# Kernel optimization log

Measured on AMD Instinct MI355X. Metric: run time of the kernel, lower is better.

The kernel has to match this reference:

```python
import jax, jax.numpy as jnp
import numpy as np


def _ramp_filter(sino):
    # Ram-Lak ramp filter along detector columns (last axis), applied in Fourier
    # space. Equivalent to projector.filter_projections, vectorized over batch.
    n = sino.shape[-1]
    ramp = (2.0 * jnp.abs(jnp.fft.fftfreq(n))).astype(sino.dtype)  # [C]
    f = jnp.fft.fft(sino, axis=-1)
    return jnp.real(jnp.fft.ifft(f * ramp, axis=-1)).astype(sino.dtype)


def _fbp(sino):
    # sino: [B, V, R, C] -> image [B, R, C, C]
    B, V, R, C = sino.shape
    filt = _ramp_filter(sino)
    npix = C
    half = (npix - 1) / 2.0
    coords = jnp.arange(npix, dtype=sino.dtype) - half
    X = coords[None, :]          # image x, broadcasts to [npix, npix]
    Y = coords[:, None]          # image y
    angles = jnp.linspace(0.0, np.pi, V, endpoint=False).astype(sino.dtype)
    dcenter = (C - 1) / 2.0

    def body(acc, inputs):
        proj, theta = inputs                      # proj: [B, R, C]
        t = X * jnp.cos(theta) + Y * jnp.sin(theta) + dcenter  # [npix, npix]
        t = jnp.clip(t, 0.0, C - 1)
        i0 = jnp.floor(t).astype(jnp.int32)
        i1 = jnp.minimum(i0 + 1, C - 1)
        w = (t - i0).astype(proj.dtype)
        g0 = proj[:, :, i0]                       # gather -> [B, R, npix, npix]
        g1 = proj[:, :, i1]
        return acc + g0 * (1.0 - w) + g1 * w, None

    init = jnp.zeros((B, R, npix, npix), sino.dtype)
    projT = jnp.moveaxis(filt, 1, 0)              # [V, B, R, C]
    acc, _ = jax.lax.scan(body, init, (projT, angles))
    img = acc * (np.pi / V)
    return jnp.maximum(img, 0.0)                  # img[img < 0] = 0


def setup_inputs() -> dict:
    key = jax.random.key(0)
    B, V, R, C = 2, 180, 32, 512
    sino = jax.random.normal(key, (B, V, R, C), dtype=jnp.float32)
    return {"sino": sino}


def reference(sino):
    return _fbp(sino)
```

## Files before the change

### kernel.cpp

```cpp
#include <hip/hip_runtime.h>
#include <hip/hip_fp16.h>
#include <math.h>

#ifndef M_PI
#define M_PI 3.14159265358979323846
#endif

#define BB 2
#define VV 180
#define RR 32
#define CC 512
#define NPIX 512

#define PADL 106
#define PW 724
#define TCEN 362

#define SH3 8
#define CHP 2
#define NCHP 45

#define SH 16
#define CH2 6
#define NCHUNK2 30

#define H4_OFF 2048
#define TAB_OFF 6144
#define FILT_OFF 2048

__global__ void precompute_kernel(float* __restrict__ ws) {
    int j = blockIdx.x * blockDim.x + threadIdx.x;
    if (j < 512) {
        float s = 0.f;
        for (int m = 1; m < 512; ++m) {
            int p = (m * j) & 511;
            float ang = (float)(2.0 * M_PI / 512.0) * (float)p;
            int mm = m < 512 - m ? m : 512 - m;
            float ramp = 2.0f * (float)mm * (1.0f / 512.0f);
            s += ramp * cosf(ang);
        }
        s *= (1.0f / 512.0f);
        s *= (float)(M_PI / (double)VV);
        ws[j] = s;
        ws[j + 512] = s;
    }
    if (j < VV) {
        float th = (float)((double)j * M_PI / 180.0);
        float c = cosf(th), sn = sinf(th);
        ws[1024 + j] = c;
        ws[1024 + 180 + j] = sn;
        ws[1408 + 2 * j] = c;
        ws[1408 + 2 * j + 1] = sn;
    }
}

__global__ void precompute_h4_kernel(float* __restrict__ ws) {
    int x = blockIdx.x * blockDim.x + threadIdx.x;
    if (x < 1024) {
        float4 h4;
        h4.x = ws[x];
        h4.y = ws[(x - 1) & 1023];
        h4.z = ws[(x - 2) & 1023];
        h4.w = ws[(x - 3) & 1023];
        *(float4*)(ws + H4_OFF + 4 * x) = h4;
    }
}

__global__ __launch_bounds__(128) void conv_table_kernel(const float* __restrict__ sino,
                                                         const float* __restrict__ ws,
                                                         unsigned int* __restrict__ table) {
    __shared__ float rows_s[16 * 512];
    __shared__ float4 h4_s[1024];
    int t = threadIdx.x;
    int blk = blockIdx.x;
    int bv = blk >> 1;
    int half = blk & 1;
    int b = bv / 180;
    int v = bv - b * 180;

    const float4* src4 = (const float4*)(sino + (((size_t)bv * 32) + (size_t)half * 16) * 512);
    float4* rows4 = (float4*)rows_s;
    for (int i = t; i < 2048; i += 128) rows4[i] = src4[i];
    const float4* h4g = (const float4*)(ws + H4_OFF);
    for (int i = t; i < 1024; i += 128) h4_s[i] = h4g[i];
    __syncthreads();

    int wave = t >> 6;
    int lane = t & 63;
    int row0 = wave * 8;

    float acc[8][8];
#pragma unroll
    for (int j = 0; j < 8; ++j)
#pragma unroll
        for (int i = 0; i < 8; ++i) acc[j][i] = 0.f;

    for (int k = 0; k < 512; k += 4) {
        float4 rv[8];
#pragma unroll
        for (int j = 0; j < 8; ++j)
            rv[j] = *(const float4*)&rows_s[(row0 + j) * 512 + k];
        float4 hq[8];
#pragma unroll
        for (int i = 0; i < 8; ++i)
            hq[i] = h4_s[lane - k + 512 + 64 * i];
#pragma unroll
        for (int j = 0; j < 8; ++j) {
#pragma unroll
            for (int i = 0; i < 8; ++i) {
                float a = acc[j][i];
                a = fmaf(rv[j].x, hq[i].x, a);
                a = fmaf(rv[j].y, hq[i].y, a);
                a = fmaf(rv[j].z, hq[i].z, a);
                a = fmaf(rv[j].w, hq[i].w, a);
                acc[j][i] = a;
            }
        }
    }

    __syncthreads();
#pragma unroll
    for (int j = 0; j < 8; ++j)
#pragma unroll
        for (int i = 0; i < 8; ++i)
            rows_s[(row0 + j) * 512 + lane + 64 * i] = acc[j][i];
    __syncthreads();

    int p = (v < 90) ? v : v - 90;
    int word = (v < 90) ? 0 : 1;
    for (int jj = 0; jj < 16; ++jj) {
        const float* fr = rows_s + jj * 512;
        int slice = b * 32 + half * 16 + jj;
        unsigned int* trow = table + (((size_t)slice * 90 + p) * PW) * 2 + word;
        for (int cx = t; cx < PW; cx += 128) {
            int s0 = cx - PADL;
            int i0 = min(max(s0, 0), 511);
            int i1 = min(max(s0 + 1, 0), 511);
            float f0 = fr[i0];
            float f1 = fr[i1];
            __half h0 = __float2half_rn(f0);
            __half h1 = __float2half_rn(f1);
            __half hd = __float2half_rn(__half2float(h1) - __half2float(h0));
            unsigned int packed = ((unsigned int)__half_as_ushort(hd) << 16) |
                                  (unsigned int)__half_as_ushort(h0);
            trow[(size_t)cx * 2] = packed;
        }
    }
}

static __device__ inline float2 unpack_h2(unsigned int u) {
    __half2 h = *reinterpret_cast<__half2*>(&u);
    return __half22float2(h);
}

__global__ __launch_bounds__(256, 6) void backproj_pair_kernel(const uint2* __restrict__ tab,
                                                               const float2* __restrict__ trigp,
                                                               float* __restrict__ out) {
    __shared__ uint2 pbuf[CHP * PW];
    __shared__ float2 trig_s[90];
    int t = threadIdx.x;
    int slice = blockIdx.y;
    int strip = blockIdx.x;
    int y0 = strip * SH3;
    const uint2* tslice = tab + (size_t)slice * (90 * PW);

    for (int i = t; i < 90; i += 256) trig_s[i] = trigp[i];

    float xc = (float)t + 0.5f;

    float acc0[SH3], acc1[SH3], acc2[SH3], acc3[SH3];
#pragma unroll
    for (int j = 0; j < SH3; ++j) { acc0[j] = 0.f; acc1[j] = 0.f; acc2[j] = 0.f; acc3[j] = 0.f; }

    for (int chunk = 0; chunk < NCHP; ++chunk) {
        __syncthreads();
        const float4* src = (const float4*)(tslice + chunk * (CHP * PW));
        float4* dst = (float4*)pbuf;
        for (int i = t; i < (CHP * PW) / 2; i += 256) dst[i] = src[i];
        __syncthreads();
#pragma unroll
        for (int pa = 0; pa < CHP; ++pa) {
            float2 cs = trig_s[chunk * CHP + pa];
            const uint2* pb = pbuf + pa * PW + TCEN;
#pragma unroll
            for (int j = 0; j < SH3; ++j) {
                float ycj = (float)(y0 + j) + 0.5f;
                float ysm  = fmaf(ycj, cs.y, -0.5f);
                float yccm = fmaf(-ycj, cs.x, -0.5f);
                float ua  = fmaf(xc, cs.x, ysm);
                float ub  = fmaf(xc, cs.y, yccm);
                float fla = floorf(ua);
                float flb = floorf(ub);
                int ma  = (int)fla;
                int mb  = (int)flb;
                float ra = ua - fla;
                float rb = ub - flb;
                int mma = -2 - ma;
                int mmb = -2 - mb;
                float rma = 1.0f - ra;
                float rmb = 1.0f - rb;
                uint2 qa  = pb[ma];
                uint2 qma = pb[mma];
                uint2 qb  = pb[mb];
                uint2 qmb = pb[mmb];
                float2 av  = unpack_h2(qa.x);
                float2 aw  = unpack_h2(qa.y);
                acc0[j] += fmaf(ra,  av.y, av.x);
                acc1[j] += fmaf(ra,  aw.y, aw.x);
                float2 mav = unpack_h2(qma.x);
                float2 maw = unpack_h2(qma.y);
                acc2[j] += fmaf(rma, mav.y, mav.x);
                acc3[j] += fmaf(rma, maw.y, maw.x);
                float2 bv  = unpack_h2(qb.x);
                float2 bw  = unpack_h2(qb.y);
                acc1[j] += fmaf(rb,  bv.y, bv.x);
                acc2[j] += fmaf(rb,  bw.y, bw.x);
                float2 mbv = unpack_h2(qmb.x);
                float2 mbw = unpack_h2(qmb.y);
                acc3[j] += fmaf(rmb, mbv.y, mbv.x);
                acc0[j] += fmaf(rmb, mbw.y, mbw.x);
            }
        }
    }

    int px = 256 + t;
    size_t sbase = (size_t)slice * (512 * 512);
#pragma unroll
    for (int j = 0; j < SH3; ++j) {
        int py = 256 + y0 + j;
        float v0 = acc0[j], v1 = acc1[j], v2 = acc2[j], v3 = acc3[j];
        out[sbase + (size_t)py * 512 + px]                   = v0 > 0.f ? v0 : 0.f;
        out[sbase + (size_t)px * 512 + (511 - py)]           = v1 > 0.f ? v1 : 0.f;
        out[sbase + (size_t)(511 - py) * 512 + (511 - px)]   = v2 > 0.f ? v2 : 0.f;
        out[sbase + (size_t)(511 - px) * 512 + py]           = v3 > 0.f ? v3 : 0.f;
    }
}

__global__ __launch_bounds__(128) void conv_kernel(const float* __restrict__ sino,
                                                   const float* __restrict__ ws,
                                                   float* __restrict__ filt) {
    __shared__ float rows_s[16 * 512];
    __shared__ float h_s[1024];
    int t = threadIdx.x;
    int blk = blockIdx.x;
    int bv = blk >> 1;
    int half = blk & 1;
    int b = bv / 180;
    int v = bv - b * 180;

    const float4* src4 = (const float4*)(sino + (((size_t)bv * 32) + (size_t)half * 16) * 512);
    float4* rows4 = (float4*)rows_s;
    for (int i = t; i < 2048; i += 128) rows4[i] = src4[i];
    for (int i = t; i < 1024; i += 128) h_s[i] = ws[i];
    __syncthreads();

    int wave = t >> 6;
    int lane = t & 63;
    int row0 = wave * 8;

    float acc[8][8];
#pragma unroll
    for (int j = 0; j < 8; ++j)
#pragma unroll
        for (int i = 0; i < 8; ++i) acc[j][i] = 0.f;

    for (int k = 0; k < 512; k += 4) {
        float4 rv[8];
#pragma unroll
        for (int j = 0; j < 8; ++j)
            rv[j] = *(const float4*)&rows_s[(row0 + j) * 512 + k];
#pragma unroll
        for (int u = 0; u < 4; ++u) {
            float hv[8];
            int base = lane - (k + u) + 512;
#pragma unroll
            for (int i = 0; i < 8; ++i) hv[i] = h_s[base + 64 * i];
#pragma unroll
            for (int j = 0; j < 8; ++j) {
                float rj = (u == 0) ? rv[j].x : (u == 1) ? rv[j].y : (u == 2) ? rv[j].z : rv[j].w;
#pragma unroll
                for (int i = 0; i < 8; ++i) acc[j][i] = fmaf(rj, hv[i], acc[j][i]);
            }
        }
    }

#pragma unroll
    for (int j = 0; j < 8; ++j) {
        int r = half * 16 + row0 + j;
        float* dst = filt + (((size_t)b * 32 + r) * 180 + v) * 512;
#pragma unroll
        for (int i = 0; i < 8; ++i) dst[lane + 64 * i] = acc[j][i];
    }
}

__global__ __launch_bounds__(256) void backproj_kernel(const float* __restrict__ filt,
                                                       const float* __restrict__ trig,
                                                       float* __restrict__ out) {
    __shared__ float2 pbuf[CH2][PW];
    __shared__ float trig_s[360];
    int t = threadIdx.x;
    int slice = blockIdx.y;
    int strip = blockIdx.x;
    int y0 = strip * SH;
    int lane = t & 63;
    int wave = t >> 6;
    int x0 = wave * 128;
    const float* slice_p = filt + (size_t)slice * (180 * 512);

    for (int i = t; i < 360; i += 256) trig_s[i] = trig[i];

    float xc0 = (float)(x0 + lane) - 255.5f;
    float xc1 = xc0 + 64.0f;
    float yb0 = (float)y0 - 255.5f;

    float acc[2][SH];
#pragma unroll
    for (int g = 0; g < 2; ++g)
#pragma unroll
        for (int j = 0; j < SH; ++j) acc[g][j] = 0.f;

    for (int chunk = 0; chunk < NCHUNK2; ++chunk) {
        int v0 = chunk * CH2;
        __syncthreads();
#pragma unroll 1
        for (int a = 0; a < CH2; ++a) {
            const float* prow = slice_p + (v0 + a) * 512;
            for (int cx = t; cx < PW; cx += 256) {
                int s0 = cx - PADL;
                int i0 = min(max(s0, 0), 511);
                int i1 = min(max(s0 + 1, 0), 511);
                float f0 = prow[i0];
                float d = prow[i1] - f0;
                float m = (float)(cx - TCEN);
                pbuf[a][cx] = make_float2(fmaf(-m, d, f0), d);
            }
        }
        __syncthreads();
#pragma unroll 1
        for (int a = 0; a < CH2; ++a) {
            float cth = trig_s[v0 + a];
            float sth = trig_s[180 + v0 + a];
            float ybase = fmaf(yb0, sth, 255.5f + (float)PADL - (float)TCEN);
            float t0 = fmaf(xc0, cth, ybase);
            float t1 = fmaf(xc1, cth, ybase);
            const char* pb = (const char*)pbuf;
            int aoff = a * (PW * 8) + TCEN * 8;
#pragma unroll
            for (int j = 0; j < SH; ++j) {
                int m0 = (int)floorf(t0);
                float2 g0 = *(const float2*)(pb + (m0 * 8 + aoff));
                acc[0][j] = fmaf(t0, g0.y, acc[0][j]) + g0.x;
                t0 += sth;

                int m1 = (int)floorf(t1);
                float2 g1 = *(const float2*)(pb + (m1 * 8 + aoff));
                acc[1][j] = fmaf(t1, g1.y, acc[1][j]) + g1.x;
                t1 += sth;
            }
        }
    }

    size_t obase = ((size_t)slice * 512 + (size_t)y0) * 512;
#pragma unroll
    for (int j = 0; j < SH; ++j) {
        float v0o = acc[0][j];
        float v1o = acc[1][j];
        out[obase + (size_t)j * 512 + x0 + lane] = v0o > 0.f ? v0o : 0.f;
        out[obase + (size_t)j * 512 + x0 + 64 + lane] = v1o > 0.f ? v1o : 0.f;
    }
}

extern "C" void kernel_launch(void* const* d_in, const int* in_sizes, int n_in,
                              void* d_out, int out_size, void* d_ws, size_t ws_size,
                              hipStream_t stream) {
    const float* sino = (const float*)d_in[0];
    float* out = (float*)d_out;
    float* ws = (float*)d_ws;

    size_t tableWords = (size_t)64 * 90 * PW * 2;
    size_t needed = ((size_t)TAB_OFF + tableWords) * 4;

    precompute_kernel<<<2, 256, 0, stream>>>(ws);
    if (ws_size >= needed) {
        unsigned int* table = (unsigned int*)(ws + TAB_OFF);
        precompute_h4_kernel<<<4, 256, 0, stream>>>(ws);
        conv_table_kernel<<<720, 128, 0, stream>>>(sino, ws, table);
        backproj_pair_kernel<<<dim3(32, 64), 256, 0, stream>>>((const uint2*)table,
                                                               (const float2*)(ws + 1408), out);
    } else {
        float* filt = ws + FILT_OFF;
        conv_kernel<<<720, 128, 0, stream>>>(sino, ws, filt);
        backproj_kernel<<<dim3(32, 64), 256, 0, stream>>>(filt, ws + 1024, out);
    }
}
```

Baseline: 682.1 us.

## Repack half table layout for packed FMA and widen conv block

Changes the half-precision table layout so each uint2 holds the two angles' base values in one word and their deltas in the other. The backprojection inner loop can then use two-wide packed FMAs (v_pk_fma_f32) with split accumulators, which are recombined once at output. The conv-table kernel moves from 128 to 256 threads with 4 rows per wave, which raises parallelism and cuts register pressure. Table writes become 16-bit scattered stores, which may cost more write bandwidth.

After: 1.100 ms. 61.3% more time.

```diff
diff --git a/kernel.cpp b/kernel.cpp
--- a/kernel.cpp
+++ b/kernel.cpp
@@ -27,6 +27,23 @@
 #define H4_OFF 2048
 #define TAB_OFF 6144
 #define FILT_OFF 2048
+
+typedef float f32x2 __attribute__((ext_vector_type(2)));
+
+static __device__ __forceinline__ f32x2 mk2(float a, float b) {
+    f32x2 r; r.x = a; r.y = b; return r;
+}
+
+static __device__ __forceinline__ float2 unpack_h2(unsigned int u) {
+    __half2 h = *reinterpret_cast<__half2*>(&u);
+    return __half22float2(h);
+}
+
+static __device__ __forceinline__ f32x2 sample2(float r, uint2 q) {
+    float2 f0 = unpack_h2(q.x);
+    float2 d  = unpack_h2(q.y);
+    return __builtin_elementwise_fma(mk2(r, r), mk2(d.x, d.y), mk2(f0.x, f0.y));
+}
 
 __global__ void precompute_kernel(float* __restrict__ ws) {
     int j = blockIdx.x * blockDim.x + threadIdx.x;
@@ -66,7 +83,7 @@
     }
 }
 
-__global__ __launch_bounds__(128) void conv_table_kernel(const float* __restrict__ sino,
+__global__ __launch_bounds__(256) void conv_table_kernel(const float* __restrict__ sino,
                                                          const float* __restrict__ ws,
                                                          unsigned int* __restrict__ table) {
     __shared__ float rows_s[16 * 512];
@@ -80,32 +97,32 @@
 
     const float4* src4 = (const float4*)(sino + (((size_t)bv * 32) + (size_t)half * 16) * 512);
     float4* rows4 = (float4*)rows_s;
-    for (int i = t; i < 2048; i += 128) rows4[i] = src4[i];
+    for (int i = t; i < 2048; i += 256) rows4[i] = src4[i];
     const float4* h4g = (const float4*)(ws + H4_OFF);
-    for (int i = t; i < 1024; i += 128) h4_s[i] = h4g[i];
+    for (int i = t; i < 1024; i += 256) h4_s[i] = h4g[i];
     __syncthreads();
 
     int wave = t >> 6;
     int lane = t & 63;
-    int row0 = wave * 8;
-
-    float acc[8][8];
-#pragma unroll
-    for (int j = 0; j < 8; ++j)
+    int row0 = wave * 4;
+
+    float acc[4][8];
+#pragma unroll
+    for (int j = 0; j < 4; ++j)
 #pragma unroll
         for (int i = 0; i < 8; ++i) acc[j][i] = 0.f;
 
     for (int k = 0; k < 512; k += 4) {
-        float4 rv[8];
-#pragma unroll
-        for (int j = 0; j < 8; ++j)
+        float4 rv[4];
+#pragma unroll
+        for (int j = 0; j < 4; ++j)
             rv[j] = *(const float4*)&rows_s[(row0 + j) * 512 + k];
         float4 hq[8];
 #pragma unroll
         for (int i = 0; i < 8; ++i)
             hq[i] = h4_s[lane - k + 512 + 64 * i];
 #pragma unroll
-        for (int j = 0; j < 8; ++j) {
+        for (int j = 0; j < 4; ++j) {
 #pragma unroll
             for (int i = 0; i < 8; ++i) {
                 float a = acc[j][i];
@@ -120,19 +137,19 @@
 
     __syncthreads();
 #pragma unroll
-    for (int j = 0; j < 8; ++j)
+    for (int j = 0; j < 4; ++j)
 #pragma unroll
         for (int i = 0; i < 8; ++i)
             rows_s[(row0 + j) * 512 + lane + 64 * i] = acc[j][i];
     __syncthreads();
 
     int p = (v < 90) ? v : v - 90;
-    int word = (v < 90) ? 0 : 1;
+    int sh = (v < 90) ? 0 : 1;
     for (int jj = 0; jj < 16; ++jj) {
         const float* fr = rows_s + jj * 512;
         int slice = b * 32 + half * 16 + jj;
-        unsigned int* trow = table + (((size_t)slice * 90 + p) * PW) * 2 + word;
-        for (int cx = t; cx < PW; cx += 128) {
+        unsigned short* trow = (unsigned short*)(table + (((size_t)slice * 90 + p) * PW) * 2);
+        for (int cx = t; cx < PW; cx += 256) {
             int s0 = cx - PADL;
             int i0 = min(max(s0, 0), 511);
             int i1 = min(max(s0 + 1, 0), 511);
@@ -141,16 +158,10 @@
             __half h0 = __float2half_rn(f0);
             __half h1 = __float2half_rn(f1);
             __half hd = __float2half_rn(__half2float(h1) - __half2float(h0));
-            unsigned int packed = ((unsigned int)__half_as_ushort(hd) << 16) |
-                                  (unsigned int)__half_as_ushort(h0);
-            trow[(size_t)cx * 2] = packed;
-        }
-    }
-}
-
-static __device__ inline float2 unpack_h2(unsigned int u) {
-    __half2 h = *reinterpret_cast<__half2*>(&u);
-    return __half22float2(h);
+            trow[(size_t)cx * 4 + sh]     = __half_as_ushort(h0);
+            trow[(size_t)cx * 4 + 2 + sh] = __half_as_ushort(hd);
+        }
+    }
 }
 
 __global__ __launch_bounds__(256, 6) void backproj_pair_kernel(const uint2* __restrict__ tab,
@@ -168,9 +179,12 @@
 
     float xc = (float)t + 0.5f;
 
-    float acc0[SH3], acc1[SH3], acc2[SH3], acc3[SH3];
-#pragma unroll
-    for (int j = 0; j < SH3; ++j) { acc0[j] = 0.f; acc1[j] = 0.f; acc2[j] = 0.f; acc3[j] = 0.f; }
+    f32x2 accA[SH3], accM[SH3], accB[SH3], accC[SH3];
+#pragma unroll
+    for (int j = 0; j < SH3; ++j) {
+        accA[j] = mk2(0.f, 0.f); accM[j] = mk2(0.f, 0.f);
+        accB[j] = mk2(0.f, 0.f); accC[j] = mk2(0.f, 0.f);
+    }
 
     for (int chunk = 0; chunk < NCHP; ++chunk) {
         __syncthreads();
@@ -203,22 +217,10 @@
                 uint2 qma = pb[mma];
                 uint2 qb  = pb[mb];
                 uint2 qmb = pb[mmb];
-                float2 av  = unpack_h2(qa.x);
-                float2 aw  = unpack_h2(qa.y);
-                acc0[j] += fmaf(ra,  av.y, av.x);
-                acc1[j] += fmaf(ra,  aw.y, aw.x);
-                float2 mav = unpack_h2(qma.x);
-                float2 maw = unpack_h2(qma.y);
-                acc2[j] += fmaf(rma, mav.y, mav.x);
-                acc3[j] += fmaf(rma, maw.y, maw.x);
-                float2 bv  = unpack_h2(qb.x);
-                float2 bw  = unpack_h2(qb.y);
-                acc1[j] += fmaf(rb,  bv.y, bv.x);
-                acc2[j] += fmaf(rb,  bw.y, bw.x);
-                float2 mbv = unpack_h2(qmb.x);
-                float2 mbw = unpack_h2(qmb.y);
-                acc3[j] += fmaf(rmb, mbv.y, mbv.x);
-                acc0[j] += fmaf(rmb, mbw.y, mbw.x);
+                accA[j] += sample2(ra,  qa);
+                accM[j] += sample2(rma, qma);
+                accB[j] += sample2(rb,  qb);
+                accC[j] += sample2(rmb, qmb);
             }
         }
     }
@@ -228,7 +230,10 @@
 #pragma unroll
     for (int j = 0; j < SH3; ++j) {
         int py = 256 + y0 + j;
-        float v0 = acc0[j], v1 = acc1[j], v2 = acc2[j], v3 = acc3[j];
+        float v0 = accA[j].x + accC[j].y;
+        float v1 = accA[j].y + accB[j].x;
+        float v2 = accM[j].x + accB[j].y;
+        float v3 = accM[j].y + accC[j].x;
         out[sbase + (size_t)py * 512 + px]                   = v0 > 0.f ? v0 : 0.f;
         out[sbase + (size_t)px * 512 + (511 - py)]           = v1 > 0.f ? v1 : 0.f;
         out[sbase + (size_t)(511 - py) * 512 + (511 - px)]   = v2 > 0.f ? v2 : 0.f;
@@ -384,7 +389,7 @@
     if (ws_size >= needed) {
         unsigned int* table = (unsigned int*)(ws + TAB_OFF);
         precompute_h4_kernel<<<4, 256, 0, stream>>>(ws);
-        conv_table_kernel<<<720, 128, 0, stream>>>(sino, ws, table);
+        conv_table_kernel<<<720, 256, 0, stream>>>(sino, ws, table);
         backproj_pair_kernel<<<dim3(32, 64), 256, 0, stream>>>((const uint2*)table,
                                                                (const float2*)(ws + 1408), out);
     } else {
```
